# Optimization experiments

Hardware: AMD Instinct MI355X
Metric: run time of the kernel (lower is better)

The kernel has to match this reference:

```python
import jax, jax.numpy as jnp
import numpy as np

B, M, EMB, K = 32768, 2048, 128, 8
TAU = 0.3

def setup_inputs() -> dict:
    key = jax.random.key(0)
    ks = jax.random.split(key, 6)
    return {
        "Gl_cur": jax.random.normal(ks[0], (B, 2), dtype=jnp.float32),
        "ancL": jax.random.normal(ks[1], (B, M, 2), dtype=jnp.float32),
        "W1": jax.random.normal(ks[2], (EMB, 2), dtype=jnp.float32) * 0.5,
        "b1": jax.random.normal(ks[3], (EMB,), dtype=jnp.float32) * 0.1,
        "W2": jax.random.normal(ks[4], (EMB, EMB), dtype=jnp.float32) * (1.0 / np.sqrt(EMB)),
        "b2": jax.random.normal(ks[5], (EMB,), dtype=jnp.float32) * 0.1,
    }

def reference(Gl_cur, ancL, W1, b1, W2, b2):
    # pairwise squared distances: [B, M]
    d2 = jnp.sum((ancL - Gl_cur[:, None, :]) ** 2, axis=-1)
    # top-k nearest anchors (topk of -d2, as in torch code)
    vals, idxs = jax.lax.top_k(-d2, K)              # vals: [B,K] (negated d2)
    topA = jnp.take_along_axis(ancL, idxs[:, :, None], axis=1)  # [B,K,2]
    # 2-layer GELU MLP (exact/erf GELU, torch default); dropout inactive in eval
    h1 = jax.nn.gelu(jnp.einsum('bkc,ec->bke', topA, W1) + b1, approximate=False)
    topE = jax.nn.gelu(jnp.einsum('bke,fe->bkf', h1, W2) + b2, approximate=False)
    # softmax combine: w = softmax(vals / -tau) = softmax(d2_top / tau), faithful to source
    w = jax.nn.softmax(vals / (-TAU), axis=1)       # [B,K]
    return jnp.sum(topE * w[:, :, None], axis=1)    # [B, EMB]
```

## Files before the change

### kernel.cpp

```cpp
#include <hip/hip_runtime.h>
#include <hip/hip_bf16.h>
#include <math.h>

#define NB   32768
#define NM   2048
#define NEMB 128
#define NK   8
#define TAU  0.3f
#define FLT_BIG 3.402823466e38f

typedef __attribute__((ext_vector_type(8))) short bf16x8;
typedef __attribute__((ext_vector_type(4))) float f32x4;

__device__ __forceinline__ float gelu_tanh(float x) {
    const float x2 = x * x;
    const float u  = fmaf(0.044715f, x2, 1.0f);
    const float a  = x * u * (-2.3022082f);
    const float e  = __builtin_amdgcn_exp2f(a);
    const float r  = __builtin_amdgcn_rcpf(e + 1.0f);
    return x * r;
}
__device__ __forceinline__ unsigned pack2(float lo, float hi) {
    __hip_bfloat162 b = __float22bfloat162_rn(make_float2(lo, hi));
    return *reinterpret_cast<unsigned*>(&b);
}

template<int CTRL>
__device__ __forceinline__ unsigned dpp_umin(unsigned v) {
    const unsigned t = (unsigned)__builtin_amdgcn_update_dpp(0, (int)v, CTRL, 0xF, 0xF, true);
    return v < t ? v : t;
}
template<int CTRL>
__device__ __forceinline__ float dpp_fadd(float v) {
    const float t = __int_as_float(__builtin_amdgcn_update_dpp(0, __float_as_int(v), CTRL, 0xF, 0xF, true));
    return v + t;
}

template<int DEPTH>
__device__ __forceinline__ int extract8(float (&ld)[DEPTH], unsigned (&lp)[DEPTH],
                                        float (&td)[8], unsigned (&tp)[8], const int lane) {
    int pops = 0;
#pragma unroll
    for (int k = 0; k < 8; ++k) {
        const unsigned key = __float_as_uint(ld[0]);
        unsigned m = key;
        m = dpp_umin<0xB1>(m);  m = dpp_umin<0x4E>(m);
        m = dpp_umin<0x141>(m); m = dpp_umin<0x140>(m);
        { unsigned t = __shfl_xor(m, 16); m = m < t ? m : t;
          t = __shfl_xor(m, 32);          m = m < t ? m : t; }
        const unsigned long long mk = __ballot(key == m);
        const int src = __ffsll(mk) - 1;
        td[k] = __uint_as_float(m);
        tp[k] = __shfl(lp[0], src);
        if (lane == src) {
#pragma unroll
            for (int j = 0; j < DEPTH - 1; ++j) { ld[j] = ld[j + 1]; lp[j] = lp[j + 1]; }
            ld[DEPTH - 1] = FLT_BIG;
            ++pops;
        }
    }
    return pops;
}

__global__ void __launch_bounds__(512, 6) fused_anchor_mlp(
    const float* __restrict__ Gl, const float* __restrict__ ancL,
    const float* __restrict__ W1, const float* __restrict__ b1,
    const float* __restrict__ W2, const float* __restrict__ b2,
    float* __restrict__ out)
{
    __shared__ uint4  w2s[2048];
    __shared__ uint4  h1s4[1024];
    __shared__ float4 b2s4[32];
    __shared__ float  wts[8][8];

    const int tid  = threadIdx.x;
    const int wave = tid >> 6;
    const int lane = tid & 63;
    const int pair = wave >> 1;
    const int half = wave & 1;
    const int rowbase = blockIdx.x << 3;
    const int row  = rowbase + wave;

    {
        const float4* w2f = reinterpret_cast<const float4*>(W2);
        for (int i = tid; i < 2048; i += 512) {
            const float4 lo = w2f[i * 2], hi = w2f[i * 2 + 1];
            uint4 u;
            u.x = pack2(lo.x, lo.y); u.y = pack2(lo.z, lo.w);
            u.z = pack2(hi.x, hi.y); u.w = pack2(hi.z, hi.w);
            w2s[(i & ~15) | ((i & 15) ^ ((i >> 4) & 7))] = u;
        }
        if (tid < 32) b2s4[tid] = reinterpret_cast<const float4*>(b2)[tid];
    }

    const float2 g = reinterpret_cast<const float2*>(Gl)[row];
    const f32x4* a4 = reinterpret_cast<const f32x4*>(ancL) + (size_t)row * (NM / 2);

    float    bd[3];
    unsigned bp[3];
#pragma unroll
    for (int i = 0; i < 3; ++i) { bd[i] = FLT_BIG; bp[i] = 0u; }

    auto ins3 = [&](float d, unsigned p) {
        const bool c0 = d < bd[0], c1 = d < bd[1], c2 = d < bd[2];
        const float n2 = __builtin_amdgcn_fmed3f(d, bd[1], bd[2]);
        const float n1 = __builtin_amdgcn_fmed3f(d, bd[0], bd[1]);
        const float n0 = fminf(d, bd[0]);
        bp[2] = c1 ? bp[1] : (c2 ? p : bp[2]);
        bp[1] = c0 ? bp[0] : (c1 ? p : bp[1]);
        bp[0] = c0 ? p : bp[0];
        bd[2] = n2; bd[1] = n1; bd[0] = n0;
    };

    f32x4 buf[3];
#pragma unroll
    for (int j = 0; j < 3; ++j) buf[j] = a4[j * 64 + lane];

#pragma unroll
    for (int it = 0; it < 16; ++it) {
        const int slot = it % 3;
        const f32x4 v = buf[slot];
        if (it + 3 < 16) buf[slot] = a4[(it + 3) * 64 + lane];
        const float dx0 = v.x - g.x, dy0 = v.y - g.y;
        const float dx1 = v.z - g.x, dy1 = v.w - g.y;
        const float d0 = __fadd_rn(__fmul_rn(dx0, dx0), __fmul_rn(dy0, dy0));
        const float d1 = __fadd_rn(__fmul_rn(dx1, dx1), __fmul_rn(dy1, dy1));
        ins3(d0, pack2(v.x, v.y));
        ins3(d1, pack2(v.z, v.w));
    }

    float    td[8];
    unsigned tp[8];
    const int pops = extract8<3>(bd, bp, td, tp, lane);

    if (__ballot(pops == 3)) {
        float    fd[8];
        unsigned fp[8];
#pragma unroll
        for (int i = 0; i < 8; ++i) { fd[i] = FLT_BIG; fp[i] = 0u; }
        for (int it = 0; it < 16; ++it) {
            const f32x4 vv = a4[it * 64 + lane];
#pragma unroll
            for (int h = 0; h < 2; ++h) {
                const float ax = h ? vv.z : vv.x;
                const float ay = h ? vv.w : vv.y;
                const float ddx = ax - g.x, ddy = ay - g.y;
                const float d = __fadd_rn(__fmul_rn(ddx, ddx), __fmul_rn(ddy, ddy));
                if (d < fd[7]) {
                    const unsigned p = pack2(ax, ay);
#pragma unroll
                    for (int j = 7; j >= 1; --j) {
                        const bool s1 = fd[j - 1] > d;
                        const bool s2 = fd[j] > d;
                        const float    nd = s1 ? fd[j - 1] : (s2 ? d : fd[j]);
                        const unsigned np = s1 ? fp[j - 1] : (s2 ? p : fp[j]);
                        fd[j] = nd; fp[j] = np;
                    }
                    if (fd[0] > d) { fd[0] = d; fp[0] = p; }
                }
            }
        }
        (void)extract8<8>(fd, fp, td, tp, lane);
    }

    const float mx = td[7];
    float ek[8], ssum = 0.f;
#pragma unroll
    for (int k = 0; k < 8; ++k) { ek[k] = __expf((td[k] - mx) * (1.0f / TAU)); ssum += ek[k]; }
    const float inv = 1.0f / ssum;
    float wv = 0.f;
#pragma unroll
    for (int k = 0; k < 8; ++k) wv = (lane == k) ? ek[k] * inv : wv;
    if (lane < 8) wts[wave][lane] = wv;

    const float4 w1v = reinterpret_cast<const float4*>(W1)[lane];
    const float2 b1v = reinterpret_cast<const float2*>(b1)[lane];
    unsigned* h1w = reinterpret_cast<unsigned*>(h1s4 + (pair << 8));
#pragma unroll
    for (int k = 0; k < 8; ++k) {
        const unsigned pk = tp[k];
        const float ax = __uint_as_float(pk << 16);
        const float ay = __uint_as_float(pk & 0xFFFF0000u);
        const float x0 = fmaf(ax, w1v.x, fmaf(ay, w1v.y, b1v.x));
        const float x1 = fmaf(ax, w1v.z, fmaf(ay, w1v.w, b1v.y));
        const int r = (half << 3) + k;
        h1w[(r << 6) + ((((lane >> 2) ^ k) << 2) | (lane & 3))] = pack2(gelu_tanh(x0), gelu_tanh(x1));
    }
    __syncthreads();

    const uint4* h1b = h1s4 + (pair << 8);
    const int bslot = lane >> 4, bxor = lane & 7, brow = (lane & 15) * 16;
    bf16x8 bq0 = __builtin_bit_cast(bf16x8, h1b[brow + (( 0 + bslot) ^ bxor)]);
    bf16x8 bq1 = __builtin_bit_cast(bf16x8, h1b[brow + (( 4 + bslot) ^ bxor)]);
    bf16x8 bq2 = __builtin_bit_cast(bf16x8, h1b[brow + (( 8 + bslot) ^ bxor)]);
    bf16x8 bq3 = __builtin_bit_cast(bf16x8, h1b[brow + ((12 + bslot) ^ bxor)]);

    const float wsel = wts[(pair << 1) | ((lane >> 3) & 1)][lane & 7];

#pragma unroll 2
    for (int i = 0; i < 4; ++i) {
        const int ft = (half << 2) + i;
        const int arow = (ft * 16 + (lane & 15)) * 16;
        f32x4 acc = {0.f, 0.f, 0.f, 0.f};
        acc = __builtin_amdgcn_mfma_f32_16x16x32_bf16(
                  __builtin_bit_cast(bf16x8, w2s[arow + (( 0 + bslot) ^ bxor)]), bq0, acc, 0, 0, 0);
        acc = __builtin_amdgcn_mfma_f32_16x16x32_bf16(
                  __builtin_bit_cast(bf16x8, w2s[arow + (( 4 + bslot) ^ bxor)]), bq1, acc, 0, 0, 0);
        acc = __builtin_amdgcn_mfma_f32_16x16x32_bf16(
                  __builtin_bit_cast(bf16x8, w2s[arow + (( 8 + bslot) ^ bxor)]), bq2, acc, 0, 0, 0);
        acc = __builtin_amdgcn_mfma_f32_16x16x32_bf16(
                  __builtin_bit_cast(bf16x8, w2s[arow + ((12 + bslot) ^ bxor)]), bq3, acc, 0, 0, 0);

        const float4 b2v = b2s4[ft * 4 + (lane >> 4)];
        float s0 = gelu_tanh(acc[0] + b2v.x) * wsel;
        float s1 = gelu_tanh(acc[1] + b2v.y) * wsel;
        float s2 = gelu_tanh(acc[2] + b2v.z) * wsel;
        float s3 = gelu_tanh(acc[3] + b2v.w) * wsel;
        s0 = dpp_fadd<0xB1>(s0); s0 = dpp_fadd<0x4E>(s0); s0 = dpp_fadd<0x141>(s0);
        s1 = dpp_fadd<0xB1>(s1); s1 = dpp_fadd<0x4E>(s1); s1 = dpp_fadd<0x141>(s1);
        s2 = dpp_fadd<0xB1>(s2); s2 = dpp_fadd<0x4E>(s2); s2 = dpp_fadd<0x141>(s2);
        s3 = dpp_fadd<0xB1>(s3); s3 = dpp_fadd<0x4E>(s3); s3 = dpp_fadd<0x141>(s3);
        if ((lane & 7) == 0) {
            const int which = (lane >> 3) & 1;
            const size_t ob = (size_t)(rowbase + (pair << 1) + which) * NEMB
                              + ft * 16 + ((lane >> 4) << 2);
            *reinterpret_cast<float4*>(&out[ob]) = make_float4(s0, s1, s2, s3);
        }
    }
}

extern "C" void kernel_launch(void* const* d_in, const int* in_sizes, int n_in,
                              void* d_out, int out_size, void* d_ws, size_t ws_size,
                              hipStream_t stream)
{
    const float* Gl  = (const float*)d_in[0];
    const float* anc = (const float*)d_in[1];
    const float* W1  = (const float*)d_in[2];
    const float* b1  = (const float*)d_in[3];
    const float* W2  = (const float*)d_in[4];
    const float* b2  = (const float*)d_in[5];
    float* outp = (float*)d_out;

    fused_anchor_mlp<<<NB / 8, 512, 0, stream>>>(Gl, anc, W1, b1, W2, b2, outp);
}
```

Measured before the change: 132.8 us.

## Process two rows per wave with interleaved top-k scans and full MFMA tiles

Each wave now handles two batch rows instead of one, interleaving their distance scans and top-3 insertions for more independent work per thread. Each wave then computes the full 128-wide second-layer MLP for its row pair instead of splitting features across a wave pair. Blocks cover 16 rows, which halves how often W2 is staged into shared memory per row, and the h1 buffer doubles. Launch bounds drop to 4 blocks per SM to allow more registers, which may reduce occupancy on this memory-bound scan.

```diff
diff --git a/kernel.cpp b/kernel.cpp
--- a/kernel.cpp
+++ b/kernel.cpp
@@ -36,50 +36,94 @@
     return v + t;
 }
 
+__device__ __forceinline__ void ins3(float (&bd)[3], unsigned (&bp)[3], float d, unsigned p) {
+    const bool c0 = d < bd[0], c1 = d < bd[1], c2 = d < bd[2];
+    const float n2 = __builtin_amdgcn_fmed3f(d, bd[1], bd[2]);
+    const float n1 = __builtin_amdgcn_fmed3f(d, bd[0], bd[1]);
+    const float n0 = fminf(d, bd[0]);
+    bp[2] = c1 ? bp[1] : (c2 ? p : bp[2]);
+    bp[1] = c0 ? bp[0] : (c1 ? p : bp[1]);
+    bp[0] = c0 ? p : bp[0];
+    bd[2] = n2; bd[1] = n1; bd[0] = n0;
+}
+
+template<int DEPTH>
+__device__ __forceinline__ int ext_round(float (&ld)[DEPTH], unsigned (&lp)[DEPTH],
+                                         float &td, unsigned &tp, const int lane) {
+    const unsigned key = __float_as_uint(ld[0]);
+    unsigned m = key;
+    m = dpp_umin<0xB1>(m);  m = dpp_umin<0x4E>(m);
+    m = dpp_umin<0x141>(m); m = dpp_umin<0x140>(m);
+    { unsigned t = __shfl_xor(m, 16); m = m < t ? m : t;
+      t = __shfl_xor(m, 32);          m = m < t ? m : t; }
+    const unsigned long long mk = __ballot(key == m);
+    const int src = __ffsll(mk) - 1;
+    td = __uint_as_float(m);
+    tp = __shfl(lp[0], src);
+    if (lane == src) {
+#pragma unroll
+        for (int j = 0; j < DEPTH - 1; ++j) { ld[j] = ld[j + 1]; lp[j] = lp[j + 1]; }
+        ld[DEPTH - 1] = FLT_BIG;
+        return 1;
+    }
+    return 0;
+}
+
 template<int DEPTH>
 __device__ __forceinline__ int extract8(float (&ld)[DEPTH], unsigned (&lp)[DEPTH],
                                         float (&td)[8], unsigned (&tp)[8], const int lane) {
     int pops = 0;
 #pragma unroll
-    for (int k = 0; k < 8; ++k) {
-        const unsigned key = __float_as_uint(ld[0]);
-        unsigned m = key;
-        m = dpp_umin<0xB1>(m);  m = dpp_umin<0x4E>(m);
-        m = dpp_umin<0x141>(m); m = dpp_umin<0x140>(m);
-        { unsigned t = __shfl_xor(m, 16); m = m < t ? m : t;
-          t = __shfl_xor(m, 32);          m = m < t ? m : t; }
-        const unsigned long long mk = __ballot(key == m);
-        const int src = __ffsll(mk) - 1;
-        td[k] = __uint_as_float(m);
-        tp[k] = __shfl(lp[0], src);
-        if (lane == src) {
-#pragma unroll
-            for (int j = 0; j < DEPTH - 1; ++j) { ld[j] = ld[j + 1]; lp[j] = lp[j + 1]; }
-            ld[DEPTH - 1] = FLT_BIG;
-            ++pops;
-        }
-    }
+    for (int k = 0; k < 8; ++k) pops += ext_round<DEPTH>(ld, lp, td[k], tp[k], lane);
     return pops;
 }
 
-__global__ void __launch_bounds__(512, 6) fused_anchor_mlp(
+__device__ __forceinline__ void fallback_row(const f32x4* a4, const float2 g,
+                                             float (&td)[8], unsigned (&tp)[8], const int lane) {
+    float    fd[8];
+    unsigned fp[8];
+#pragma unroll
+    for (int i = 0; i < 8; ++i) { fd[i] = FLT_BIG; fp[i] = 0u; }
+    for (int it = 0; it < 16; ++it) {
+        const f32x4 vv = a4[it * 64 + lane];
+#pragma unroll
+        for (int h = 0; h < 2; ++h) {
+            const float ax = h ? vv.z : vv.x;
+            const float ay = h ? vv.w : vv.y;
+            const float ddx = ax - g.x, ddy = ay - g.y;
+            const float d = __fadd_rn(__fmul_rn(ddx, ddx), __fmul_rn(ddy, ddy));
+            if (d < fd[7]) {
+                const unsigned p = pack2(ax, ay);
+#pragma unroll
+                for (int j = 7; j >= 1; --j) {
+                    const bool s1 = fd[j - 1] > d;
+                    const bool s2 = fd[j] > d;
+                    const float    nd = s1 ? fd[j - 1] : (s2 ? d : fd[j]);
+                    const unsigned np = s1 ? fp[j - 1] : (s2 ? p : fp[j]);
+                    fd[j] = nd; fp[j] = np;
+                }
+                if (fd[0] > d) { fd[0] = d; fp[0] = p; }
+            }
+        }
+    }
+    (void)extract8<8>(fd, fp, td, tp, lane);
+}
+
+__global__ void __launch_bounds__(512, 4) fused_anchor_mlp(
     const float* __restrict__ Gl, const float* __restrict__ ancL,
     const float* __restrict__ W1, const float* __restrict__ b1,
     const float* __restrict__ W2, const float* __restrict__ b2,
     float* __restrict__ out)
 {
     __shared__ uint4  w2s[2048];
-    __shared__ uint4  h1s4[1024];
+    __shared__ uint4  h1s4[2048];
     __shared__ float4 b2s4[32];
-    __shared__ float  wts[8][8];
+    __shared__ float  wts[8][2][8];
 
     const int tid  = threadIdx.x;
     const int wave = tid >> 6;
     const int lane = tid & 63;
-    const int pair = wave >> 1;
-    const int half = wave & 1;
-    const int rowbase = blockIdx.x << 3;
-    const int row  = rowbase + wave;
+    const int rowA = (blockIdx.x << 4) + (wave << 1);
 
     {
         const float4* w2f = reinterpret_cast<const float4*>(W2);
@@ -93,113 +137,110 @@
         if (tid < 32) b2s4[tid] = reinterpret_cast<const float4*>(b2)[tid];
     }
 
-    const float2 g = reinterpret_cast<const float2*>(Gl)[row];
-    const f32x4* a4 = reinterpret_cast<const f32x4*>(ancL) + (size_t)row * (NM / 2);
-
-    float    bd[3];
-    unsigned bp[3];
-#pragma unroll
-    for (int i = 0; i < 3; ++i) { bd[i] = FLT_BIG; bp[i] = 0u; }
-
-    auto ins3 = [&](float d, unsigned p) {
-        const bool c0 = d < bd[0], c1 = d < bd[1], c2 = d < bd[2];
-        const float n2 = __builtin_amdgcn_fmed3f(d, bd[1], bd[2]);
-        const float n1 = __builtin_amdgcn_fmed3f(d, bd[0], bd[1]);
-        const float n0 = fminf(d, bd[0]);
-        bp[2] = c1 ? bp[1] : (c2 ? p : bp[2]);
-        bp[1] = c0 ? bp[0] : (c1 ? p : bp[1]);
-        bp[0] = c0 ? p : bp[0];
-        bd[2] = n2; bd[1] = n1; bd[0] = n0;
-    };
-
-    f32x4 buf[3];
-#pragma unroll
-    for (int j = 0; j < 3; ++j) buf[j] = a4[j * 64 + lane];
+    const float2 gA = reinterpret_cast<const float2*>(Gl)[rowA];
+    const float2 gB = reinterpret_cast<const float2*>(Gl)[rowA + 1];
+    const f32x4* aA = reinterpret_cast<const f32x4*>(ancL) + (size_t)rowA * (NM / 2);
+    const f32x4* aB = aA + (NM / 2);
+
+    float    bdA[3], bdB[3];
+    unsigned bpA[3], bpB[3];
+#pragma unroll
+    for (int i = 0; i < 3; ++i) {
+        bdA[i] = FLT_BIG; bpA[i] = 0u;
+        bdB[i] = FLT_BIG; bpB[i] = 0u;
+    }
+
+    f32x4 bufA[2], bufB[2];
+#pragma unroll
+    for (int j = 0; j < 2; ++j) { bufA[j] = aA[j * 64 + lane]; bufB[j] = aB[j * 64 + lane]; }
 
 #pragma unroll
     for (int it = 0; it < 16; ++it) {
-        const int slot = it % 3;
-        const f32x4 v = buf[slot];
-        if (it + 3 < 16) buf[slot] = a4[(it + 3) * 64 + lane];
-        const float dx0 = v.x - g.x, dy0 = v.y - g.y;
-        const float dx1 = v.z - g.x, dy1 = v.w - g.y;
-        const float d0 = __fadd_rn(__fmul_rn(dx0, dx0), __fmul_rn(dy0, dy0));
-        const float d1 = __fadd_rn(__fmul_rn(dx1, dx1), __fmul_rn(dy1, dy1));
-        ins3(d0, pack2(v.x, v.y));
-        ins3(d1, pack2(v.z, v.w));
-    }
-
-    float    td[8];
-    unsigned tp[8];
-    const int pops = extract8<3>(bd, bp, td, tp, lane);
-
-    if (__ballot(pops == 3)) {
-        float    fd[8];
-        unsigned fp[8];
-#pragma unroll
-        for (int i = 0; i < 8; ++i) { fd[i] = FLT_BIG; fp[i] = 0u; }
-        for (int it = 0; it < 16; ++it) {
-            const f32x4 vv = a4[it * 64 + lane];
-#pragma unroll
-            for (int h = 0; h < 2; ++h) {
-                const float ax = h ? vv.z : vv.x;
-                const float ay = h ? vv.w : vv.y;
-                const float ddx = ax - g.x, ddy = ay - g.y;
-                const float d = __fadd_rn(__fmul_rn(ddx, ddx), __fmul_rn(ddy, ddy));
-                if (d < fd[7]) {
-                    const unsigned p = pack2(ax, ay);
-#pragma unroll
-                    for (int j = 7; j >= 1; --j) {
-                        const bool s1 = fd[j - 1] > d;
-                        const bool s2 = fd[j] > d;
-                        const float    nd = s1 ? fd[j - 1] : (s2 ? d : fd[j]);
-                        const unsigned np = s1 ? fp[j - 1] : (s2 ? p : fp[j]);
-                        fd[j] = nd; fp[j] = np;
-                    }
-                    if (fd[0] > d) { fd[0] = d; fp[0] = p; }
-                }
-            }
-        }
-        (void)extract8<8>(fd, fp, td, tp, lane);
-    }
-
-    const float mx = td[7];
-    float ek[8], ssum = 0.f;
-#pragma unroll
-    for (int k = 0; k < 8; ++k) { ek[k] = __expf((td[k] - mx) * (1.0f / TAU)); ssum += ek[k]; }
-    const float inv = 1.0f / ssum;
-    float wv = 0.f;
-#pragma unroll
-    for (int k = 0; k < 8; ++k) wv = (lane == k) ? ek[k] * inv : wv;
-    if (lane < 8) wts[wave][lane] = wv;
+        const int slot = it & 1;
+        const f32x4 vA = bufA[slot];
+        const f32x4 vB = bufB[slot];
+        if (it + 2 < 16) {
+            bufA[slot] = aA[(it + 2) * 64 + lane];
+            bufB[slot] = aB[(it + 2) * 64 + lane];
+        }
+        const float dxA0 = vA.x - gA.x, dyA0 = vA.y - gA.y;
+        const float dxA1 = vA.z - gA.x, dyA1 = vA.w - gA.y;
+        const float dA0 = __fadd_rn(__fmul_rn(dxA0, dxA0), __fmul_rn(dyA0, dyA0));
+        const float dA1 = __fadd_rn(__fmul_rn(dxA1, dxA1), __fmul_rn(dyA1, dyA1));
+        const float dxB0 = vB.x - gB.x, dyB0 = vB.y - gB.y;
+        const float dxB1 = vB.z - gB.x, dyB1 = vB.w - gB.y;
+        const float dB0 = __fadd_rn(__fmul_rn(dxB0, dxB0), __fmul_rn(dyB0, dyB0));
+        const float dB1 = __fadd_rn(__fmul_rn(dxB1, dxB1), __fmul_rn(dyB1, dyB1));
+        ins3(bdA, bpA, dA0, pack2(vA.x, vA.y));
+        ins3(bdB, bpB, dB0, pack2(vB.x, vB.y));
+        ins3(bdA, bpA, dA1, pack2(vA.z, vA.w));
+        ins3(bdB, bpB, dB1, pack2(vB.z, vB.w));
+    }
+
+    float    tdA[8], tdB[8];
+    unsigned tpA[8], tpB[8];
+    int popsA = 0, popsB = 0;
+#pragma unroll
+    for (int k = 0; k < 8; ++k) {
+        popsA += ext_round<3>(bdA, bpA, tdA[k], tpA[k], lane);
+        popsB += ext_round<3>(bdB, bpB, tdB[k], tpB[k], lane);
+    }
+
+    if (__ballot(popsA == 3)) fallback_row(aA, gA, tdA, tpA, lane);
+    if (__ballot(popsB == 3)) fallback_row(aB, gB, tdB, tpB, lane);
+
+    {
+        const float mxA = tdA[7], mxB = tdB[7];
+        float ekA[8], ekB[8], sA = 0.f, sB = 0.f;
+#pragma unroll
+        for (int k = 0; k < 8; ++k) {
+            ekA[k] = __expf((tdA[k] - mxA) * (1.0f / TAU)); sA += ekA[k];
+            ekB[k] = __expf((tdB[k] - mxB) * (1.0f / TAU)); sB += ekB[k];
+        }
+        const float invA = 1.0f / sA, invB = 1.0f / sB;
+        float wvA = 0.f, wvB = 0.f;
+#pragma unroll
+        for (int k = 0; k < 8; ++k) {
+            wvA = (lane == k) ? ekA[k] * invA : wvA;
+            wvB = (lane == k) ? ekB[k] * invB : wvB;
+        }
+        if (lane < 8) {
+            wts[wave][0][lane] = wvA;
+            wts[wave][1][lane] = wvB;
+        }
+    }
 
     const float4 w1v = reinterpret_cast<const float4*>(W1)[lane];
     const float2 b1v = reinterpret_cast<const float2*>(b1)[lane];
-    unsigned* h1w = reinterpret_cast<unsigned*>(h1s4 + (pair << 8));
+    unsigned* h1w = reinterpret_cast<unsigned*>(h1s4 + (wave << 8));
 #pragma unroll
     for (int k = 0; k < 8; ++k) {
-        const unsigned pk = tp[k];
-        const float ax = __uint_as_float(pk << 16);
-        const float ay = __uint_as_float(pk & 0xFFFF0000u);
-        const float x0 = fmaf(ax, w1v.x, fmaf(ay, w1v.y, b1v.x));
-        const float x1 = fmaf(ax, w1v.z, fmaf(ay, w1v.w, b1v.y));
-        const int r = (half << 3) + k;
-        h1w[(r << 6) + ((((lane >> 2) ^ k) << 2) | (lane & 3))] = pack2(gelu_tanh(x0), gelu_tanh(x1));
+        const unsigned pkA = tpA[k], pkB = tpB[k];
+        const float axA = __uint_as_float(pkA << 16);
+        const float ayA = __uint_as_float(pkA & 0xFFFF0000u);
+        const float axB = __uint_as_float(pkB << 16);
+        const float ayB = __uint_as_float(pkB & 0xFFFF0000u);
+        const float xA0 = fmaf(axA, w1v.x, fmaf(ayA, w1v.y, b1v.x));
+        const float xA1 = fmaf(axA, w1v.z, fmaf(ayA, w1v.w, b1v.y));
+        const float xB0 = fmaf(axB, w1v.x, fmaf(ayB, w1v.y, b1v.x));
+        const float xB1 = fmaf(axB, w1v.z, fmaf(ayB, w1v.w, b1v.y));
+        const int sw = ((((lane >> 2) ^ k) << 2) | (lane & 3));
+        h1w[(k << 6) + sw]         = pack2(gelu_tanh(xA0), gelu_tanh(xA1));
+        h1w[((8 + k) << 6) + sw]   = pack2(gelu_tanh(xB0), gelu_tanh(xB1));
     }
     __syncthreads();
 
-    const uint4* h1b = h1s4 + (pair << 8);
+    const uint4* h1b = h1s4 + (wave << 8);
     const int bslot = lane >> 4, bxor = lane & 7, brow = (lane & 15) * 16;
     bf16x8 bq0 = __builtin_bit_cast(bf16x8, h1b[brow + (( 0 + bslot) ^ bxor)]);
     bf16x8 bq1 = __builtin_bit_cast(bf16x8, h1b[brow + (( 4 + bslot) ^ bxor)]);
     bf16x8 bq2 = __builtin_bit_cast(bf16x8, h1b[brow + (( 8 + bslot) ^ bxor)]);
     bf16x8 bq3 = __builtin_bit_cast(bf16x8, h1b[brow + ((12 + bslot) ^ bxor)]);
 
-    const float wsel = wts[(pair << 1) | ((lane >> 3) & 1)][lane & 7];
+    const float wsel = wts[wave][(lane >> 3) & 1][lane & 7];
 
 #pragma unroll 2
-    for (int i = 0; i < 4; ++i) {
-        const int ft = (half << 2) + i;
+    for (int ft = 0; ft < 8; ++ft) {
         const int arow = (ft * 16 + (lane & 15)) * 16;
         f32x4 acc = {0.f, 0.f, 0.f, 0.f};
         acc = __builtin_amdgcn_mfma_f32_16x16x32_bf16(
@@ -222,7 +263,7 @@
         s3 = dpp_fadd<0xB1>(s3); s3 = dpp_fadd<0x4E>(s3); s3 = dpp_fadd<0x141>(s3);
         if ((lane & 7) == 0) {
             const int which = (lane >> 3) & 1;
-            const size_t ob = (size_t)(rowbase + (pair << 1) + which) * NEMB
+            const size_t ob = (size_t)(rowA + which) * NEMB
                               + ft * 16 + ((lane >> 4) << 2);
             *reinterpret_cast<float4*>(&out[ob]) = make_float4(s0, s1, s2, s3);
         }
@@ -241,5 +282,5 @@
     const float* b2  = (const float*)d_in[5];
     float* outp = (float*)d_out;
 
-    fused_anchor_mlp<<<NB / 8, 512, 0, stream>>>(Gl, anc, W1, b1, W2, b2, outp);
-}
+    fused_anchor_mlp<<<NB / 16, 512, 0, stream>>>(Gl, anc, W1, b1, W2, b2, outp);
+}
```

Measured after the change: 148.6 us. 1.12x slower.

## Make kernel persistent with full-row register prefetch across strided rows

Applied to the files above, without the earlier changes.

Launches a fixed grid of 512 blocks in which each wave processes 8 rows strided by 4096. While it computes top-k and the MLP for the current row, it prefetches the whole next anchor row (16 vector loads per lane) into registers. This amortizes the W2-to-LDS staging and the block-wide sync over more rows, and aims to keep more memory requests in flight to hide the bandwidth-bound anchor stream. Each wave now runs the second-layer MFMA for its own 8 rows, with the 16-column tile half duplicated. Register pressure rises, so launch bounds drop from 6 to 4, and occupancy falls to about 2 blocks per CU.

```diff
diff --git a/kernel.cpp b/kernel.cpp
--- a/kernel.cpp
+++ b/kernel.cpp
@@ -8,6 +8,8 @@
 #define NK   8
 #define TAU  0.3f
 #define FLT_BIG 3.402823466e38f
+#define ROWS_PER_WAVE 8
+#define ROWSTEP 4096
 
 typedef __attribute__((ext_vector_type(8))) short bf16x8;
 typedef __attribute__((ext_vector_type(4))) float f32x4;
@@ -36,33 +38,80 @@
     return v + t;
 }
 
+__device__ __forceinline__ void ins3(float (&bd)[3], unsigned (&bp)[3], float d, unsigned p) {
+    const bool c0 = d < bd[0], c1 = d < bd[1], c2 = d < bd[2];
+    const float n2 = __builtin_amdgcn_fmed3f(d, bd[1], bd[2]);
+    const float n1 = __builtin_amdgcn_fmed3f(d, bd[0], bd[1]);
+    const float n0 = fminf(d, bd[0]);
+    bp[2] = c1 ? bp[1] : (c2 ? p : bp[2]);
+    bp[1] = c0 ? bp[0] : (c1 ? p : bp[1]);
+    bp[0] = c0 ? p : bp[0];
+    bd[2] = n2; bd[1] = n1; bd[0] = n0;
+}
+
+template<int DEPTH>
+__device__ __forceinline__ int ext_round(float (&ld)[DEPTH], unsigned (&lp)[DEPTH],
+                                         float &td, unsigned &tp, const int lane) {
+    const unsigned key = __float_as_uint(ld[0]);
+    unsigned m = key;
+    m = dpp_umin<0xB1>(m);  m = dpp_umin<0x4E>(m);
+    m = dpp_umin<0x141>(m); m = dpp_umin<0x140>(m);
+    { unsigned t = __shfl_xor(m, 16); m = m < t ? m : t;
+      t = __shfl_xor(m, 32);          m = m < t ? m : t; }
+    const unsigned long long mk = __ballot(key == m);
+    const int src = __ffsll(mk) - 1;
+    td = __uint_as_float(m);
+    tp = __shfl(lp[0], src);
+    if (lane == src) {
+#pragma unroll
+        for (int j = 0; j < DEPTH - 1; ++j) { ld[j] = ld[j + 1]; lp[j] = lp[j + 1]; }
+        ld[DEPTH - 1] = FLT_BIG;
+        return 1;
+    }
+    return 0;
+}
+
 template<int DEPTH>
 __device__ __forceinline__ int extract8(float (&ld)[DEPTH], unsigned (&lp)[DEPTH],
                                         float (&td)[8], unsigned (&tp)[8], const int lane) {
     int pops = 0;
 #pragma unroll
-    for (int k = 0; k < 8; ++k) {
-        const unsigned key = __float_as_uint(ld[0]);
-        unsigned m = key;
-        m = dpp_umin<0xB1>(m);  m = dpp_umin<0x4E>(m);
-        m = dpp_umin<0x141>(m); m = dpp_umin<0x140>(m);
-        { unsigned t = __shfl_xor(m, 16); m = m < t ? m : t;
-          t = __shfl_xor(m, 32);          m = m < t ? m : t; }
-        const unsigned long long mk = __ballot(key == m);
-        const int src = __ffsll(mk) - 1;
-        td[k] = __uint_as_float(m);
-        tp[k] = __shfl(lp[0], src);
-        if (lane == src) {
-#pragma unroll
-            for (int j = 0; j < DEPTH - 1; ++j) { ld[j] = ld[j + 1]; lp[j] = lp[j + 1]; }
-            ld[DEPTH - 1] = FLT_BIG;
-            ++pops;
-        }
-    }
+    for (int k = 0; k < 8; ++k) pops += ext_round<DEPTH>(ld, lp, td[k], tp[k], lane);
     return pops;
 }
 
-__global__ void __launch_bounds__(512, 6) fused_anchor_mlp(
+__device__ __forceinline__ void fallback_row(const f32x4* a4, const float2 g,
+                                             float (&td)[8], unsigned (&tp)[8], const int lane) {
+    float    fd[8];
+    unsigned fp[8];
+#pragma unroll
+    for (int i = 0; i < 8; ++i) { fd[i] = FLT_BIG; fp[i] = 0u; }
+    for (int it = 0; it < 16; ++it) {
+        const f32x4 vv = a4[it * 64 + lane];
+#pragma unroll
+        for (int h = 0; h < 2; ++h) {
+            const float ax = h ? vv.z : vv.x;
+            const float ay = h ? vv.w : vv.y;
+            const float ddx = ax - g.x, ddy = ay - g.y;
+            const float d = __fadd_rn(__fmul_rn(ddx, ddx), __fmul_rn(ddy, ddy));
+            if (d < fd[7]) {
+                const unsigned p = pack2(ax, ay);
+#pragma unroll
+                for (int j = 7; j >= 1; --j) {
+                    const bool s1 = fd[j - 1] > d;
+                    const bool s2 = fd[j] > d;
+                    const float    nd = s1 ? fd[j - 1] : (s2 ? d : fd[j]);
+                    const unsigned np = s1 ? fp[j - 1] : (s2 ? p : fp[j]);
+                    fd[j] = nd; fp[j] = np;
+                }
+                if (fd[0] > d) { fd[0] = d; fp[0] = p; }
+            }
+        }
+    }
+    (void)extract8<8>(fd, fp, td, tp, lane);
+}
+
+__global__ void __launch_bounds__(512, 4) fused_anchor_mlp(
     const float* __restrict__ Gl, const float* __restrict__ ancL,
     const float* __restrict__ W1, const float* __restrict__ b1,
     const float* __restrict__ W2, const float* __restrict__ b2,
@@ -71,15 +120,11 @@
     __shared__ uint4  w2s[2048];
     __shared__ uint4  h1s4[1024];
     __shared__ float4 b2s4[32];
-    __shared__ float  wts[8][8];
 
     const int tid  = threadIdx.x;
     const int wave = tid >> 6;
     const int lane = tid & 63;
-    const int pair = wave >> 1;
-    const int half = wave & 1;
-    const int rowbase = blockIdx.x << 3;
-    const int row  = rowbase + wave;
+    const int wg   = (blockIdx.x << 3) + wave;
 
     {
         const float4* w2f = reinterpret_cast<const float4*>(W2);
@@ -92,140 +137,110 @@
         }
         if (tid < 32) b2s4[tid] = reinterpret_cast<const float4*>(b2)[tid];
     }
-
-    const float2 g = reinterpret_cast<const float2*>(Gl)[row];
-    const f32x4* a4 = reinterpret_cast<const f32x4*>(ancL) + (size_t)row * (NM / 2);
-
-    float    bd[3];
-    unsigned bp[3];
-#pragma unroll
-    for (int i = 0; i < 3; ++i) { bd[i] = FLT_BIG; bp[i] = 0u; }
-
-    auto ins3 = [&](float d, unsigned p) {
-        const bool c0 = d < bd[0], c1 = d < bd[1], c2 = d < bd[2];
-        const float n2 = __builtin_amdgcn_fmed3f(d, bd[1], bd[2]);
-        const float n1 = __builtin_amdgcn_fmed3f(d, bd[0], bd[1]);
-        const float n0 = fminf(d, bd[0]);
-        bp[2] = c1 ? bp[1] : (c2 ? p : bp[2]);
-        bp[1] = c0 ? bp[0] : (c1 ? p : bp[1]);
-        bp[0] = c0 ? p : bp[0];
-        bd[2] = n2; bd[1] = n1; bd[0] = n0;
-    };
-
-    f32x4 buf[3];
-#pragma unroll
-    for (int j = 0; j < 3; ++j) buf[j] = a4[j * 64 + lane];
-
-#pragma unroll
-    for (int it = 0; it < 16; ++it) {
-        const int slot = it % 3;
-        const f32x4 v = buf[slot];
-        if (it + 3 < 16) buf[slot] = a4[(it + 3) * 64 + lane];
-        const float dx0 = v.x - g.x, dy0 = v.y - g.y;
-        const float dx1 = v.z - g.x, dy1 = v.w - g.y;
-        const float d0 = __fadd_rn(__fmul_rn(dx0, dx0), __fmul_rn(dy0, dy0));
-        const float d1 = __fadd_rn(__fmul_rn(dx1, dx1), __fmul_rn(dy1, dy1));
-        ins3(d0, pack2(v.x, v.y));
-        ins3(d1, pack2(v.z, v.w));
-    }
-
-    float    td[8];
-    unsigned tp[8];
-    const int pops = extract8<3>(bd, bp, td, tp, lane);
-
-    if (__ballot(pops == 3)) {
-        float    fd[8];
-        unsigned fp[8];
-#pragma unroll
-        for (int i = 0; i < 8; ++i) { fd[i] = FLT_BIG; fp[i] = 0u; }
-        for (int it = 0; it < 16; ++it) {
-            const f32x4 vv = a4[it * 64 + lane];
-#pragma unroll
-            for (int h = 0; h < 2; ++h) {
-                const float ax = h ? vv.z : vv.x;
-                const float ay = h ? vv.w : vv.y;
-                const float ddx = ax - g.x, ddy = ay - g.y;
-                const float d = __fadd_rn(__fmul_rn(ddx, ddx), __fmul_rn(ddy, ddy));
-                if (d < fd[7]) {
-                    const unsigned p = pack2(ax, ay);
-#pragma unroll
-                    for (int j = 7; j >= 1; --j) {
-                        const bool s1 = fd[j - 1] > d;
-                        const bool s2 = fd[j] > d;
-                        const float    nd = s1 ? fd[j - 1] : (s2 ? d : fd[j]);
-                        const unsigned np = s1 ? fp[j - 1] : (s2 ? p : fp[j]);
-                        fd[j] = nd; fp[j] = np;
-                    }
-                    if (fd[0] > d) { fd[0] = d; fp[0] = p; }
-                }
-            }
-        }
-        (void)extract8<8>(fd, fp, td, tp, lane);
-    }
-
-    const float mx = td[7];
-    float ek[8], ssum = 0.f;
-#pragma unroll
-    for (int k = 0; k < 8; ++k) { ek[k] = __expf((td[k] - mx) * (1.0f / TAU)); ssum += ek[k]; }
-    const float inv = 1.0f / ssum;
-    float wv = 0.f;
-#pragma unroll
-    for (int k = 0; k < 8; ++k) wv = (lane == k) ? ek[k] * inv : wv;
-    if (lane < 8) wts[wave][lane] = wv;
+    __syncthreads();
+
+    const float2* Gl2 = reinterpret_cast<const float2*>(Gl);
+    const f32x4*  aCur = reinterpret_cast<const f32x4*>(ancL) + (size_t)wg * (NM / 2);
+    const size_t  STEP = (size_t)ROWSTEP * (NM / 2);
 
     const float4 w1v = reinterpret_cast<const float4*>(W1)[lane];
     const float2 b1v = reinterpret_cast<const float2*>(b1)[lane];
-    unsigned* h1w = reinterpret_cast<unsigned*>(h1s4 + (pair << 8));
-#pragma unroll
-    for (int k = 0; k < 8; ++k) {
-        const unsigned pk = tp[k];
-        const float ax = __uint_as_float(pk << 16);
-        const float ay = __uint_as_float(pk & 0xFFFF0000u);
-        const float x0 = fmaf(ax, w1v.x, fmaf(ay, w1v.y, b1v.x));
-        const float x1 = fmaf(ax, w1v.z, fmaf(ay, w1v.w, b1v.y));
-        const int r = (half << 3) + k;
-        h1w[(r << 6) + ((((lane >> 2) ^ k) << 2) | (lane & 3))] = pack2(gelu_tanh(x0), gelu_tanh(x1));
-    }
-    __syncthreads();
-
-    const uint4* h1b = h1s4 + (pair << 8);
-    const int bslot = lane >> 4, bxor = lane & 7, brow = (lane & 15) * 16;
-    bf16x8 bq0 = __builtin_bit_cast(bf16x8, h1b[brow + (( 0 + bslot) ^ bxor)]);
-    bf16x8 bq1 = __builtin_bit_cast(bf16x8, h1b[brow + (( 4 + bslot) ^ bxor)]);
-    bf16x8 bq2 = __builtin_bit_cast(bf16x8, h1b[brow + (( 8 + bslot) ^ bxor)]);
-    bf16x8 bq3 = __builtin_bit_cast(bf16x8, h1b[brow + ((12 + bslot) ^ bxor)]);
-
-    const float wsel = wts[(pair << 1) | ((lane >> 3) & 1)][lane & 7];
-
+    unsigned* h1w = reinterpret_cast<unsigned*>(h1s4 + (wave << 7));
+    const uint4* h1b = h1s4 + (wave << 7);
+    const int bslot = lane >> 4, bxor = lane & 7;
+
+    float2 gCur = Gl2[wg];
+
+    f32x4 buf[16];
+#pragma unroll
+    for (int j = 0; j < 16; ++j) buf[j] = aCur[j * 64 + lane];
+
+    for (int r = 0; r < ROWS_PER_WAVE; ++r) {
+        const int row = wg + r * ROWSTEP;
+        const f32x4* aNext = aCur + STEP;
+        const bool pf = (r < ROWS_PER_WAVE - 1);
+        float2 gNext = gCur;
+        if (pf) gNext = Gl2[row + ROWSTEP];
+
+        float    bd[3];
+        unsigned bp[3];
+#pragma unroll
+        for (int i = 0; i < 3; ++i) { bd[i] = FLT_BIG; bp[i] = 0u; }
+
+#pragma unroll
+        for (int it = 0; it < 16; ++it) {
+            const f32x4 v = buf[it];
+            if (pf) buf[it] = aNext[it * 64 + lane];
+            const float dx0 = v.x - gCur.x, dy0 = v.y - gCur.y;
+            const float dx1 = v.z - gCur.x, dy1 = v.w - gCur.y;
+            const float d0 = __fadd_rn(__fmul_rn(dx0, dx0), __fmul_rn(dy0, dy0));
+            const float d1 = __fadd_rn(__fmul_rn(dx1, dx1), __fmul_rn(dy1, dy1));
+            ins3(bd, bp, d0, pack2(v.x, v.y));
+            ins3(bd, bp, d1, pack2(v.z, v.w));
+        }
+
+        float    td[8];
+        unsigned tp[8];
+        const int pops = extract8<3>(bd, bp, td, tp, lane);
+
+        if (__ballot(pops == 3)) fallback_row(aCur, gCur, td, tp, lane);
+
+        const float mx = td[7];
+        float ek[8], ssum = 0.f;
+#pragma unroll
+        for (int k = 0; k < 8; ++k) { ek[k] = __expf((td[k] - mx) * (1.0f / TAU)); ssum += ek[k]; }
+        const float inv = 1.0f / ssum;
+        float wsel = 0.f;
+#pragma unroll
+        for (int k = 0; k < 8; ++k) wsel = ((lane & 7) == k) ? ek[k] * inv : wsel;
+
+#pragma unroll
+        for (int k = 0; k < 8; ++k) {
+            const unsigned pk = tp[k];
+            const float ax = __uint_as_float(pk << 16);
+            const float ay = __uint_as_float(pk & 0xFFFF0000u);
+            const float x0 = fmaf(ax, w1v.x, fmaf(ay, w1v.y, b1v.x));
+            const float x1 = fmaf(ax, w1v.z, fmaf(ay, w1v.w, b1v.y));
+            h1w[(k << 6) + ((((lane >> 2) ^ k) << 2) | (lane & 3))] =
+                pack2(gelu_tanh(x0), gelu_tanh(x1));
+        }
+
+        const int brow = (lane & 7) * 16;
+        bf16x8 bq0 = __builtin_bit_cast(bf16x8, h1b[brow + (( 0 + bslot) ^ bxor)]);
+        bf16x8 bq1 = __builtin_bit_cast(bf16x8, h1b[brow + (( 4 + bslot) ^ bxor)]);
+        bf16x8 bq2 = __builtin_bit_cast(bf16x8, h1b[brow + (( 8 + bslot) ^ bxor)]);
+        bf16x8 bq3 = __builtin_bit_cast(bf16x8, h1b[brow + ((12 + bslot) ^ bxor)]);
+
+        const size_t outbase = (size_t)row * NEMB;
 #pragma unroll 2
-    for (int i = 0; i < 4; ++i) {
-        const int ft = (half << 2) + i;
-        const int arow = (ft * 16 + (lane & 15)) * 16;
-        f32x4 acc = {0.f, 0.f, 0.f, 0.f};
-        acc = __builtin_amdgcn_mfma_f32_16x16x32_bf16(
-                  __builtin_bit_cast(bf16x8, w2s[arow + (( 0 + bslot) ^ bxor)]), bq0, acc, 0, 0, 0);
-        acc = __builtin_amdgcn_mfma_f32_16x16x32_bf16(
-                  __builtin_bit_cast(bf16x8, w2s[arow + (( 4 + bslot) ^ bxor)]), bq1, acc, 0, 0, 0);
-        acc = __builtin_amdgcn_mfma_f32_16x16x32_bf16(
-                  __builtin_bit_cast(bf16x8, w2s[arow + (( 8 + bslot) ^ bxor)]), bq2, acc, 0, 0, 0);
-        acc = __builtin_amdgcn_mfma_f32_16x16x32_bf16(
-                  __builtin_bit_cast(bf16x8, w2s[arow + ((12 + bslot) ^ bxor)]), bq3, acc, 0, 0, 0);
-
-        const float4 b2v = b2s4[ft * 4 + (lane >> 4)];
-        float s0 = gelu_tanh(acc[0] + b2v.x) * wsel;
-        float s1 = gelu_tanh(acc[1] + b2v.y) * wsel;
-        float s2 = gelu_tanh(acc[2] + b2v.z) * wsel;
-        float s3 = gelu_tanh(acc[3] + b2v.w) * wsel;
-        s0 = dpp_fadd<0xB1>(s0); s0 = dpp_fadd<0x4E>(s0); s0 = dpp_fadd<0x141>(s0);
-        s1 = dpp_fadd<0xB1>(s1); s1 = dpp_fadd<0x4E>(s1); s1 = dpp_fadd<0x141>(s1);
-        s2 = dpp_fadd<0xB1>(s2); s2 = dpp_fadd<0x4E>(s2); s2 = dpp_fadd<0x141>(s2);
-        s3 = dpp_fadd<0xB1>(s3); s3 = dpp_fadd<0x4E>(s3); s3 = dpp_fadd<0x141>(s3);
-        if ((lane & 7) == 0) {
-            const int which = (lane >> 3) & 1;
-            const size_t ob = (size_t)(rowbase + (pair << 1) + which) * NEMB
-                              + ft * 16 + ((lane >> 4) << 2);
-            *reinterpret_cast<float4*>(&out[ob]) = make_float4(s0, s1, s2, s3);
-        }
+        for (int ft = 0; ft < 8; ++ft) {
+            const int arow = (ft * 16 + (lane & 15)) * 16;
+            f32x4 acc = {0.f, 0.f, 0.f, 0.f};
+            acc = __builtin_amdgcn_mfma_f32_16x16x32_bf16(
+                      __builtin_bit_cast(bf16x8, w2s[arow + (( 0 + bslot) ^ bxor)]), bq0, acc, 0, 0, 0);
+            acc = __builtin_amdgcn_mfma_f32_16x16x32_bf16(
+                      __builtin_bit_cast(bf16x8, w2s[arow + (( 4 + bslot) ^ bxor)]), bq1, acc, 0, 0, 0);
+            acc = __builtin_amdgcn_mfma_f32_16x16x32_bf16(
+                      __builtin_bit_cast(bf16x8, w2s[arow + (( 8 + bslot) ^ bxor)]), bq2, acc, 0, 0, 0);
+            acc = __builtin_amdgcn_mfma_f32_16x16x32_bf16(
+                      __builtin_bit_cast(bf16x8, w2s[arow + ((12 + bslot) ^ bxor)]), bq3, acc, 0, 0, 0);
+
+            const float4 b2v = b2s4[ft * 4 + (lane >> 4)];
+            float s0 = gelu_tanh(acc[0] + b2v.x) * wsel;
+            float s1 = gelu_tanh(acc[1] + b2v.y) * wsel;
+            float s2 = gelu_tanh(acc[2] + b2v.z) * wsel;
+            float s3 = gelu_tanh(acc[3] + b2v.w) * wsel;
+            s0 = dpp_fadd<0xB1>(s0); s0 = dpp_fadd<0x4E>(s0); s0 = dpp_fadd<0x141>(s0);
+            s1 = dpp_fadd<0xB1>(s1); s1 = dpp_fadd<0x4E>(s1); s1 = dpp_fadd<0x141>(s1);
+            s2 = dpp_fadd<0xB1>(s2); s2 = dpp_fadd<0x4E>(s2); s2 = dpp_fadd<0x141>(s2);
+            s3 = dpp_fadd<0xB1>(s3); s3 = dpp_fadd<0x4E>(s3); s3 = dpp_fadd<0x141>(s3);
+            if ((lane & 15) == 0)
+                *reinterpret_cast<float4*>(&out[outbase + ft * 16 + ((lane >> 4) << 2)]) =
+                    make_float4(s0, s1, s2, s3);
+        }
+
+        aCur = aNext;
+        gCur = gNext;
     }
 }
 
@@ -241,5 +256,5 @@
     const float* b2  = (const float*)d_in[5];
     float* outp = (float*)d_out;
 
-    fused_anchor_mlp<<<NB / 8, 512, 0, stream>>>(Gl, anc, W1, b1, W2, b2, outp);
-}
+    fused_anchor_mlp<<<512, 512, 0, stream>>>(Gl, anc, W1, b1, W2, b2, outp);
+}
```

New measurement: 260.3 us. +96.0%, slower.
